# Kernel tuning notes

Hardware: AMD Instinct MI355X
Metric: run time of the kernel (lower is better)

The kernel has to match this reference:

```python
import jax, jax.numpy as jnp
import numpy as np

K_NN = 32          # configs['k']
LEAKY_ALPHA = 0.2  # configs['alpha']
NHEADS = 8         # all heads share gat_W0/gat_a0 in the weights dict -> tiled output
NEG_INF = -9e15    # masked-softmax fill used by dense GAT


@jax.custom_vjp
def grad_reverse(x):
    # GradientReversalLayer: identity forward, negated gradient backward
    return x

def _gr_fwd(x):
    return x, None

def _gr_bwd(res, g):
    return (-g,)

grad_reverse.defvjp(_gr_fwd, _gr_bwd)


def setup_inputs() -> dict:
    key = jax.random.key(0)
    ks = jax.random.split(key, 11)
    N, D = 6144, 512           # N = (num_domains+1)*batch_size = 4*1536
    H1, H2, G = 256, 128, 64   # hidden_layers=[256,128], gat_hidden=[64]
    C, ND = 16, 3              # num_classes, num source-domain discriminators

    def xav(k, shape):
        limit = np.float32(np.sqrt(6.0 / (shape[0] + shape[1])) * 1.414)
        return jax.random.uniform(k, shape, jnp.float32, -limit, limit)

    return {
        "x": jax.random.normal(ks[0], (N, D), jnp.float32),
        "fc_W0": xav(ks[1], (D, H1)),
        "fc_b0": jax.random.normal(ks[2], (H1,), jnp.float32) * 0.01,
        "fc_W1": xav(ks[3], (H1, H2)),
        "fc_b1": jax.random.normal(ks[4], (H2,), jnp.float32) * 0.01,
        "gat_W": xav(ks[5], (H2, G)),
        "gat_a": jax.random.normal(ks[6], (2 * G, 1), jnp.float32) * 0.1,
        "cls_W": xav(ks[7], (NHEADS * G, C)),
        "cls_b": jax.random.normal(ks[8], (C,), jnp.float32) * 0.01,
        "dsc_W": jax.random.uniform(ks[9], (ND, NHEADS * G, 2), jnp.float32),
        "dsc_b": jax.random.uniform(ks[10], (ND, 2), jnp.float32),
    }


def reference(x, fc_W0, fc_b0, fc_W1, fc_b1, gat_W, gat_a, cls_W, cls_b, dsc_W, dsc_b):
    # --- feature extractor MLP (Linear 'fc' + relu), dropout=0 / eval mode ---
    h = jax.nn.relu(x @ fc_W0 + fc_b0)
    h = jax.nn.relu(h @ fc_W1 + fc_b1)          # [N, 128]
    n = h.shape[0]

    # --- AdjacencyLayer / DistanceLayer: kNN over pairwise L2 distances ---
    sq = jnp.sum(h * h, axis=1)
    d2 = sq[:, None] + sq[None, :] - 2.0 * (h @ h.T)      # [N, N] squared dists
    d2 = d2 + jnp.eye(n, dtype=h.dtype) * 1e9             # exclude self from kNN
    _, idx = jax.lax.top_k(-jax.lax.stop_gradient(d2), K_NN)  # [N, K]
    adj = jnp.zeros((n, n), h.dtype).at[jnp.arange(n)[:, None], idx].set(1.0)
    adj = adj + jnp.eye(n, dtype=h.dtype)                 # self loops

    # --- dense GraphAttentionLayer (single shared head, tiled nheads times) ---
    Wh = h @ gat_W                                        # [N, G]
    Gd = Wh.shape[1]
    f1 = Wh @ gat_a[:Gd]                                  # [N, 1]
    f2 = Wh @ gat_a[Gd:]                                  # [N, 1]
    e = jax.nn.leaky_relu(f1 + f2.T, LEAKY_ALPHA)         # [N, N]
    att = jax.nn.softmax(jnp.where(adj > 0, e, NEG_INF), axis=1)
    hp = jax.nn.elu(att @ Wh)                             # [N, G]
    gat_out = jnp.tile(hp, (1, NHEADS))                   # concat of shared heads

    # --- class head + domain discriminators behind gradient reversal ---
    cls_logits = gat_out @ cls_W + cls_b                  # [N, C]
    rev = grad_reverse(gat_out)
    dsc_logits = jnp.einsum('nd,kdo->nko', rev, dsc_W) + dsc_b  # [N, ND, 2]
    return jnp.concatenate([cls_logits, dsc_logits.reshape(n, -1)], axis=1)
```

## Files before the change

### kernel.cpp

```cpp
#include <hip/hip_runtime.h>
#include <float.h>

#define N_PTS 6144
#define D_IN  512
#define H1_DIM 256
#define H2_DIM 128
#define G_DIM  64
#define KNN    32
#define NOUT   22
#define NQ     (N_PTS / 4)

typedef short s8v __attribute__((ext_vector_type(8)));
typedef float f32x4 __attribute__((ext_vector_type(4)));
typedef unsigned u32x4 __attribute__((ext_vector_type(4)));
typedef unsigned short u16;
typedef unsigned short u16x4 __attribute__((ext_vector_type(4)));
typedef unsigned long long u64;

__device__ __forceinline__ u16 f2bf(float f) {
  unsigned u = __float_as_uint(f);
  u += 0x7FFFu + ((u >> 16) & 1u);
  return (u16)(u >> 16);
}
__device__ __forceinline__ float bf2f(u16 s) {
  return __uint_as_float(((unsigned)s) << 16);
}
__device__ __forceinline__ void split3(float v, u16& a0, u16& a1, u16& a2) {
  a0 = f2bf(v);
  float r1 = v - bf2f(a0);
  a1 = f2bf(r1);
  a2 = f2bf(r1 - bf2f(a1));
}
__device__ __forceinline__ unsigned sortkey(float f) {
  unsigned ub = __float_as_uint(f);
  return (ub & 0x80000000u) ? ~ub : (ub | 0x80000000u);
}

template<int BM, bool AF32, bool SPLITK, bool BIAS, bool RELU, bool WF32, bool WSPLIT>
__global__ __launch_bounds__(256, 4) void mfma_gemm(
    const void* __restrict__ A0any, const u16* __restrict__ A1_, const u16* __restrict__ A2_,
    const u16* __restrict__ B0_, const u16* __restrict__ B1_, const u16* __restrict__ B2_,
    const float* __restrict__ bias,
    float* __restrict__ Cf, u16* __restrict__ C0, u16* __restrict__ C1, u16* __restrict__ C2,
    int Ktot, int Ks, int ldC, size_t MN)
{
  const int MT = BM / 32, NT = 2;
  const int APL = BM * 32;
  const int BBASE = 3 * APL;
  __shared__ u16 lds[(BM + 64) * 32 * 3];

  const int t = threadIdx.x;
  const int lane = t & 63, wave = t >> 6;
  const int wm = wave >> 1, wn = wave & 1;
  const int m0 = blockIdx.y * BM, n0 = blockIdx.x * 64;
  const int kz = blockIdx.z * Ks;

  f32x4 acc[MT][NT] = {};

  const int pA = BM / 16;
  const int NC = 3 * pA + 12;

  for (int k0 = 0; k0 < Ks; k0 += 32) {
    if (k0) __syncthreads();
    const int kb = kz + k0;
    if (AF32) {
      const float* A = (const float*)A0any;
      #pragma unroll
      for (int c0 = 0; c0 < BM * 4; c0 += 256) {
        int c = c0 + t;
        int row = c >> 2, slot = c & 3;
        const float* g = A + (size_t)(m0 + row) * Ktot + kb + slot * 8;
        f32x4 fa = *(const f32x4*)g;
        f32x4 fb = *(const f32x4*)(g + 4);
        int dst = row * 32 + ((slot ^ ((row >> 1) & 3)) << 3);
        s8v v0, v1, v2;
        #pragma unroll
        for (int e = 0; e < 4; ++e) {
          u16 a0, a1, a2; split3(fa[e], a0, a1, a2);
          v0[e] = (short)a0; v1[e] = (short)a1; v2[e] = (short)a2;
        }
        #pragma unroll
        for (int e = 0; e < 4; ++e) {
          u16 a0, a1, a2; split3(fb[e], a0, a1, a2);
          v0[4 + e] = (short)a0; v1[4 + e] = (short)a1; v2[4 + e] = (short)a2;
        }
        *(s8v*)(lds + dst) = v0;
        *(s8v*)(lds + APL + dst) = v1;
        *(s8v*)(lds + 2 * APL + dst) = v2;
      }
      for (int c = wave; c < 12; c += 4) {
        int p = c >> 2, lc = c & 3;
        int row = lc * 16 + (lane >> 2);
        int srcslot = (lane & 3) ^ ((row >> 1) & 3);
        const u16* src = (p == 0) ? B0_ : (p == 1) ? B1_ : B2_;
        const u16* g = src + (size_t)(n0 + row) * Ktot + kb + srcslot * 8;
        __builtin_amdgcn_global_load_lds(
            (const __attribute__((address_space(1))) unsigned*)g,
            (__attribute__((address_space(3))) unsigned*)(lds + BBASE + p * 2048 + lc * 512),
            16, 0, 0);
      }
    } else {
      for (int c = wave; c < NC; c += 4) {
        const u16* src; int dstoff; int row0; int lc;
        if (c < 3 * pA) {
          int p = c / pA; lc = c % pA;
          src = (p == 0) ? (const u16*)A0any : (p == 1) ? A1_ : A2_;
          dstoff = p * APL + lc * 512;
          row0 = m0;
        } else {
          int cb = c - 3 * pA;
          int p = cb >> 2; lc = cb & 3;
          src = (p == 0) ? B0_ : (p == 1) ? B1_ : B2_;
          dstoff = BBASE + p * 2048 + lc * 512;
          row0 = n0;
        }
        int row = lc * 16 + (lane >> 2);
        int srcslot = (lane & 3) ^ ((row >> 1) & 3);
        const u16* g = src + (size_t)(row0 + row) * Ktot + kb + srcslot * 8;
        __builtin_amdgcn_global_load_lds(
            (const __attribute__((address_space(1))) unsigned*)g,
            (__attribute__((address_space(3))) unsigned*)(lds + dstoff),
            16, 0, 0);
      }
    }
    __syncthreads();

    s8v af[3][MT], bf[3][NT];
    #pragma unroll
    for (int mt = 0; mt < MT; ++mt) {
      int r = wm * (BM / 2) + mt * 16 + (lane & 15);
      int off = r * 32 + (((lane >> 4) ^ ((r >> 1) & 3)) << 3);
      #pragma unroll
      for (int p = 0; p < 3; ++p) af[p][mt] = *(const s8v*)(lds + p * APL + off);
    }
    #pragma unroll
    for (int nt = 0; nt < NT; ++nt) {
      int r = wn * 32 + nt * 16 + (lane & 15);
      int off = r * 32 + (((lane >> 4) ^ ((r >> 1) & 3)) << 3);
      #pragma unroll
      for (int p = 0; p < 3; ++p) bf[p][nt] = *(const s8v*)(lds + BBASE + p * 2048 + off);
    }
    #pragma unroll
    for (int mt = 0; mt < MT; ++mt)
      #pragma unroll
      for (int nt = 0; nt < NT; ++nt) {
        f32x4 a = acc[mt][nt];
        a = __builtin_amdgcn_mfma_f32_16x16x32_bf16(af[0][mt], bf[0][nt], a, 0, 0, 0);
        a = __builtin_amdgcn_mfma_f32_16x16x32_bf16(af[0][mt], bf[1][nt], a, 0, 0, 0);
        a = __builtin_amdgcn_mfma_f32_16x16x32_bf16(af[1][mt], bf[0][nt], a, 0, 0, 0);
        a = __builtin_amdgcn_mfma_f32_16x16x32_bf16(af[1][mt], bf[1][nt], a, 0, 0, 0);
        a = __builtin_amdgcn_mfma_f32_16x16x32_bf16(af[0][mt], bf[2][nt], a, 0, 0, 0);
        a = __builtin_amdgcn_mfma_f32_16x16x32_bf16(af[2][mt], bf[0][nt], a, 0, 0, 0);
        acc[mt][nt] = a;
      }
  }

  #pragma unroll
  for (int mt = 0; mt < MT; ++mt) {
    #pragma unroll
    for (int nt = 0; nt < NT; ++nt) {
      int col = n0 + wn * 32 + nt * 16 + (lane & 15);
      float bv = (BIAS && !SPLITK) ? bias[col] : 0.f;
      #pragma unroll
      for (int v = 0; v < 4; ++v) {
        int row = m0 + wm * (BM / 2) + mt * 16 + (lane >> 4) * 4 + v;
        float val = acc[mt][nt][v] + bv;
        size_t o = (size_t)row * ldC + col;
        if (SPLITK) {
          Cf[(size_t)blockIdx.z * MN + o] = val;
        } else {
          if (RELU) val = fmaxf(val, 0.f);
          if (WF32) Cf[o] = val;
          if (WSPLIT) {
            u16 a0, a1, a2; split3(val, a0, a1, a2);
            C0[o] = a0; C1[o] = a1; C2[o] = a2;
          }
        }
      }
    }
  }
}

__global__ __launch_bounds__(512, 4) void gram_symm(
    const u16* __restrict__ A0, const u16* __restrict__ A1, const u16* __restrict__ A2,
    const float* __restrict__ sq, u16* __restrict__ Ck, u16* __restrict__ Qm, int ldC)
{
  if ((int)blockIdx.x < (int)blockIdx.y) return;
  const int MT = 4, NT = 2;
  __shared__ u16 lds[2 * 128 * 32 * 3];

  const int t = threadIdx.x;
  const int lane = t & 63, wave = t >> 6;
  const int wm = wave >> 2, wn = wave & 3;
  const int m0 = blockIdx.y * 128, n0 = blockIdx.x * 128;
  const bool mirror = (int)blockIdx.x > (int)blockIdx.y;

  f32x4 acc[MT][NT] = {};

  for (int k0 = 0; k0 < H2_DIM; k0 += 32) {
    if (k0) __syncthreads();
    for (int c = wave; c < 48; c += 8) {
      int half = c >= 24;
      int cb = half ? c - 24 : c;
      int p = cb >> 3, lc = cb & 7;
      const u16* src = (p == 0) ? A0 : (p == 1) ? A1 : A2;
      int dstoff = half * 12288 + p * 4096 + lc * 512;
      int row0 = half ? n0 : m0;
      int row = lc * 16 + (lane >> 2);
      int srcslot = (lane & 3) ^ ((row >> 1) & 3);
      const u16* g = src + (size_t)(row0 + row) * H2_DIM + k0 + srcslot * 8;
      __builtin_amdgcn_global_load_lds(
          (const __attribute__((address_space(1))) unsigned*)g,
          (__attribute__((address_space(3))) unsigned*)(lds + dstoff),
          16, 0, 0);
    }
    __syncthreads();

    s8v af[3][MT], bf[3][NT];
    #pragma unroll
    for (int mt = 0; mt < MT; ++mt) {
      int r = wm * 64 + mt * 16 + (lane & 15);
      int off = r * 32 + (((lane >> 4) ^ ((r >> 1) & 3)) << 3);
      #pragma unroll
      for (int p = 0; p < 3; ++p) af[p][mt] = *(const s8v*)(lds + p * 4096 + off);
    }
    #pragma unroll
    for (int nt = 0; nt < NT; ++nt) {
      int r = wn * 32 + nt * 16 + (lane & 15);
      int off = r * 32 + (((lane >> 4) ^ ((r >> 1) & 3)) << 3);
      #pragma unroll
      for (int p = 0; p < 3; ++p) bf[p][nt] = *(const s8v*)(lds + 12288 + p * 4096 + off);
    }
    #pragma unroll
    for (int mt = 0; mt < MT; ++mt)
      #pragma unroll
      for (int nt = 0; nt < NT; ++nt) {
        f32x4 a = acc[mt][nt];
        a = __builtin_amdgcn_mfma_f32_16x16x32_bf16(af[0][mt], bf[0][nt], a, 0, 0, 0);
        a = __builtin_amdgcn_mfma_f32_16x16x32_bf16(af[0][mt], bf[1][nt], a, 0, 0, 0);
        a = __builtin_amdgcn_mfma_f32_16x16x32_bf16(af[1][mt], bf[0][nt], a, 0, 0, 0);
        a = __builtin_amdgcn_mfma_f32_16x16x32_bf16(af[1][mt], bf[1][nt], a, 0, 0, 0);
        a = __builtin_amdgcn_mfma_f32_16x16x32_bf16(af[0][mt], bf[2][nt], a, 0, 0, 0);
        a = __builtin_amdgcn_mfma_f32_16x16x32_bf16(af[2][mt], bf[0][nt], a, 0, 0, 0);
        acc[mt][nt] = a;
      }
  }

  unsigned mk32[MT][NT][2];
  __syncthreads();
  u16* stD = lds;
  #pragma unroll
  for (int mt = 0; mt < MT; ++mt) {
    #pragma unroll
    for (int nt = 0; nt < NT; ++nt) {
      int cl = wn * 32 + nt * 16 + (lane & 15);
      float sqc = sq[n0 + cl];
      #pragma unroll
      for (int v = 0; v < 4; ++v) {
        int rl = wm * 64 + mt * 16 + (lane >> 4) * 4 + v;
        float val = acc[mt][nt][v];
        float f = fmaf(-2.f, val, sqc);
        unsigned uu = sortkey(f);
        if (m0 + rl == n0 + cl) uu = 0xFFFFFFFFu;
        stD[rl * 136 + cl] = (u16)(uu >> 16);
        if (mirror) {
          unsigned km = sortkey(fmaf(-2.f, val, sq[m0 + rl])) >> 16;
          if (v & 1) mk32[mt][nt][v >> 1] |= km << 16;
          else       mk32[mt][nt][v >> 1] = km;
        }
      }
    }
  }
  __syncthreads();
  for (int e = t; e < 128 * 16; e += 512) {
    int row = e >> 4, ch = e & 15;
    u32x4 vv = *(const u32x4*)(stD + row * 136 + ch * 8);
    *(u32x4*)(Ck + (size_t)(m0 + row) * ldC + n0 + ch * 8) = vv;
  }
  for (int e = t; e < 128 * 32; e += 512) {
    int row = e >> 5, qg = e & 31;
    const u16* p = stD + row * 136 + qg * 4;
    u16 a = p[0] < p[1] ? p[0] : p[1];
    u16 b = p[2] < p[3] ? p[2] : p[3];
    Qm[(size_t)(m0 + row) * NQ + (n0 >> 2) + qg] = a < b ? a : b;
  }
  if (mirror) {
    __syncthreads();
    u16* stM = lds;
    #pragma unroll
    for (int mt = 0; mt < MT; ++mt) {
      #pragma unroll
      for (int nt = 0; nt < NT; ++nt) {
        int cl = wn * 32 + nt * 16 + (lane & 15);
        #pragma unroll
        for (int v = 0; v < 4; ++v) {
          int rl = wm * 64 + mt * 16 + (lane >> 4) * 4 + v;
          unsigned km = (v & 1) ? (mk32[mt][nt][v >> 1] >> 16)
                                : (mk32[mt][nt][v >> 1] & 0xFFFFu);
          stM[cl * 136 + rl] = (u16)km;
        }
      }
    }
    __syncthreads();
    for (int e = t; e < 128 * 16; e += 512) {
      int row = e >> 4, ch = e & 15;
      u32x4 vv = *(const u32x4*)(stM + row * 136 + ch * 8);
      *(u32x4*)(Ck + (size_t)(n0 + row) * ldC + m0 + ch * 8) = vv;
    }
    for (int e = t; e < 128 * 32; e += 512) {
      int row = e >> 5, qg = e & 31;
      const u16* p = stM + row * 136 + qg * 4;
      u16 a = p[0] < p[1] ? p[0] : p[1];
      u16 b = p[2] < p[3] ? p[2] : p[3];
      Qm[(size_t)(n0 + row) * NQ + (m0 >> 2) + qg] = a < b ? a : b;
    }
  }
}

template<int S, bool BIAS, bool RELU, bool WF32, bool WSPLIT>
__global__ void combine(const float* __restrict__ P, const float* __restrict__ bias,
                        size_t MN, int Ncols,
                        float* __restrict__ Cf, u16* __restrict__ C0,
                        u16* __restrict__ C1, u16* __restrict__ C2)
{
  size_t idx = ((size_t)blockIdx.x * 256 + threadIdx.x) * 4;
  if (idx >= MN) return;
  f32x4 s = *(const f32x4*)(P + idx);
  #pragma unroll
  for (int z = 1; z < S; ++z) s += *(const f32x4*)(P + (size_t)z * MN + idx);
  int n = (int)(idx % (size_t)Ncols);
  #pragma unroll
  for (int e = 0; e < 4; ++e) {
    float v = s[e] + (BIAS ? bias[n + e] : 0.f);
    if (RELU) v = fmaxf(v, 0.f);
    if (WF32) Cf[idx + e] = v;
    if (WSPLIT) {
      u16 a0, a1, a2; split3(v, a0, a1, a2);
      C0[idx + e] = a0; C1[idx + e] = a1; C2[idx + e] = a2;
    }
  }
}

__global__ void prep_all(const float* __restrict__ W0, u16* __restrict__ a0,
                         u16* __restrict__ a1, u16* __restrict__ a2,
                         const float* __restrict__ W1, u16* __restrict__ b0,
                         u16* __restrict__ b1, u16* __restrict__ b2,
                         const float* __restrict__ gW, u16* __restrict__ c0,
                         u16* __restrict__ c1, u16* __restrict__ c2,
                         const float* __restrict__ cW, const float* __restrict__ cb,
                         const float* __restrict__ dW, const float* __restrict__ db,
                         float* __restrict__ Wc, float* __restrict__ bc)
{
  int id = blockIdx.x * 256 + threadIdx.x;
  const int S0 = D_IN * H1_DIM, S1 = H1_DIM * H2_DIM, S2 = H2_DIM * G_DIM;
  const int SW = S0 + S1 + S2;
  if (id < SW) {
    const float* W; u16 *p0, *p1, *p2; int K, N;
    if (id < S0)           { W = W0; p0 = a0; p1 = a1; p2 = a2; K = D_IN;   N = H1_DIM; }
    else if (id < S0 + S1) { id -= S0; W = W1; p0 = b0; p1 = b1; p2 = b2; K = H1_DIM; N = H2_DIM; }
    else                   { id -= S0 + S1; W = gW; p0 = c0; p1 = c1; p2 = c2; K = H2_DIM; N = G_DIM; }
    int k = id / N, n = id % N;
    u16 x0, x1, x2;
    split3(W[id], x0, x1, x2);
    size_t o = (size_t)n * K + k;
    p0[o] = x0; p1[o] = x1; p2[o] = x2;
    return;
  }
  id -= SW;
  if (id < 64 * NOUT) {
    int g = id / NOUT, c = id % NOUT;
    float s = 0.f;
    if (c < 16) {
      for (int r = 0; r < 8; ++r) s += cW[(r * 64 + g) * 16 + c];
    } else {
      int k = (c - 16) >> 1, o = (c - 16) & 1;
      for (int r = 0; r < 8; ++r) s += dW[k * 1024 + (r * 64 + g) * 2 + o];
    }
    Wc[id] = s;
    if (g == 0) bc[c] = (c < 16) ? cb[c] : db[c - 16];
  }
}

__global__ void row_stats(const float* __restrict__ h, const float* __restrict__ Wh,
                          const float* __restrict__ ga, float* __restrict__ sq,
                          float* __restrict__ f1, float* __restrict__ f2)
{
  int i = blockIdx.x * 256 + threadIdx.x;
  const float* hr = h + (size_t)i * H2_DIM;
  float s = 0.f;
  for (int k = 0; k < H2_DIM; ++k) { float v = hr[k]; s = fmaf(v, v, s); }
  sq[i] = s;
  const float* wr = Wh + (size_t)i * G_DIM;
  float a = 0.f, b = 0.f;
  for (int g = 0; g < G_DIM; ++g) {
    float w = wr[g];
    a = fmaf(w, ga[g], a);
    b = fmaf(w, ga[G_DIM + g], b);
  }
  f1[i] = a; f2[i] = b;
}

__global__ __launch_bounds__(256) void topk_att(const u16* __restrict__ Sb,
    const u16* __restrict__ Qm,
    const float* __restrict__ f1, const float* __restrict__ f2,
    const float* __restrict__ Wh, const float* __restrict__ Wc, const float* __restrict__ bc,
    const float* __restrict__ sq, const float* __restrict__ hF,
    float* __restrict__ out, int m0, int nrows)
{
  const int t = threadIdx.x;
  const int lane = t & 63, wv = t >> 6;
  const int row4 = (nrows - 4 - blockIdx.x * 4) + wv;
  const int i = m0 + row4;
  const u16* Srow = Sb + (size_t)row4 * N_PTS;
  const u16* Qrow = Qm + (size_t)row4 * NQ;

  __shared__ float WcL[64 * NOUT];
  __shared__ unsigned candS[4][384];
  __shared__ u16 tieS[4][128];
  __shared__ float hiL[4][128];
  __shared__ int neighS[4][33];
  __shared__ float attS[4][33];
  __shared__ float hpfS[4][64];

  for (int idx = t; idx < 64 * NOUT; idx += 256) WcL[idx] = Wc[idx];
  __syncthreads();

  hiL[wv][lane]      = hF[(size_t)i * H2_DIM + lane];
  hiL[wv][64 + lane] = hF[(size_t)i * H2_DIM + 64 + lane];

  unsigned q[24];
  #pragma unroll
  for (int g = 0; g < 6; ++g) {
    u16x4 v = *(const u16x4*)(Qrow + (g << 8) + (lane << 2));
    #pragma unroll
    for (int e = 0; e < 4; ++e) q[g * 4 + e] = (unsigned)v[e];
  }
  #define QI(s) (((s >> 2) << 8) + (lane << 2) + (s & 3))

  unsigned lmin = q[0];
  #pragma unroll
  for (int c = 1; c < 24; ++c) lmin = q[c] < lmin ? q[c] : lmin;

  unsigned mnl = lmin, mxl = lmin;
  #pragma unroll
  for (int off = 32; off > 0; off >>= 1) {
    unsigned o1 = __shfl_xor(mnl, off); mnl = o1 < mnl ? o1 : mnl;
    unsigned o2 = __shfl_xor(mxl, off); mxl = o2 > mxl ? o2 : mxl;
  }

  long long lo = (long long)mnl - 1, hi = (long long)mxl;
  while (hi - lo > 1) {
    long long span = hi - lo;
    unsigned m1 = (unsigned)(lo + (span >> 2));
    unsigned m2 = (unsigned)(lo + (span >> 1));
    unsigned m3 = (unsigned)(hi - (span >> 2));
    int c1 = 0, c2 = 0, c3 = 0;
    #pragma unroll
    for (int c = 0; c < 24; ++c) {
      c1 += (q[c] <= m1);
      c2 += (q[c] <= m2);
      c3 += (q[c] <= m3);
    }
    #pragma unroll
    for (int off = 32; off > 0; off >>= 1) {
      c1 += __shfl_xor(c1, off);
      c2 += __shfl_xor(c2, off);
      c3 += __shfl_xor(c3, off);
    }
    if (c1 >= KNN)       { hi = m1; }
    else if (c2 >= KNN)  { lo = m1; hi = m2; }
    else if (c3 >= KNN)  { lo = m2; hi = m3; }
    else                 { lo = m3; }
  }
  const unsigned Q = (unsigned)hi;

  #pragma unroll
  for (int s = 0; s < 6; ++s) candS[wv][lane + s * 64] = 0xFFFFFFFFu;
  const u64 below = (lane == 0) ? 0ull : (~0ull >> (64 - lane));
  int qcnt = 0;
  #pragma unroll
  for (int s = 0; s < 24; ++s) {
    bool act = (q[s] <= Q);
    u64 mask = __ballot(act);
    if (act) {
      int pos = qcnt + (int)__popcll(mask & below);
      if (pos < 96) {
        int qi = QI(s);
        u16x4 v = *(const u16x4*)(Srow + (qi << 2));
        #pragma unroll
        for (int e = 0; e < 4; ++e) {
          int j = (qi << 2) + e;
          candS[wv][pos * 4 + e] = ((unsigned)v[e] << 13) | (unsigned)j;
        }
      }
    }
    qcnt += (int)__popcll(mask);
  }

  unsigned ck[6];
  #pragma unroll
  for (int s = 0; s < 6; ++s) ck[s] = candS[wv][lane + s * 64];

  lo = -1; hi = 0x10000;
  while (hi - lo > 1) {
    long long span = hi - lo;
    unsigned m1 = (unsigned)(lo + (span >> 2));
    unsigned m2 = (unsigned)(lo + (span >> 1));
    unsigned m3 = (unsigned)(hi - (span >> 2));
    int c1 = 0, c2 = 0, c3 = 0;
    #pragma unroll
    for (int s = 0; s < 6; ++s) {
      unsigned k = ck[s] >> 13;
      c1 += (k <= m1);
      c2 += (k <= m2);
      c3 += (k <= m3);
    }
    #pragma unroll
    for (int off = 32; off > 0; off >>= 1) {
      c1 += __shfl_xor(c1, off);
      c2 += __shfl_xor(c2, off);
      c3 += __shfl_xor(c3, off);
    }
    if (c1 >= KNN)       { hi = m1; }
    else if (c2 >= KNN)  { lo = m1; hi = m2; }
    else if (c3 >= KNN)  { lo = m2; hi = m3; }
    else                 { lo = m3; }
  }
  const unsigned T = (unsigned)hi;

  int sA = 0, sB = 0;
  #pragma unroll
  for (int s = 0; s < 6; ++s) {
    unsigned k = ck[s] >> 13;
    bool strict = (k < T);
    u64 ms = __ballot(strict);
    if (strict) {
      int pos = sA + (int)__popcll(ms & below);
      if (pos < 32) neighS[wv][pos] = (int)(ck[s] & 0x1FFFu);
    }
    sA += (int)__popcll(ms);
    bool tie = (k == T);
    u64 mt2 = __ballot(tie);
    if (tie) {
      int pos = sB + (int)__popcll(mt2 & below);
      if (pos < 128) tieS[wv][pos] = (u16)(ck[s] & 0x1FFFu);
    }
    sB += (int)__popcll(mt2);
  }
  if (sB > 128) sB = 128;
  const int need = KNN - sA;

  u64 r0 = ~0ull, r1 = ~0ull;
  const float* hi0 = &hiL[wv][0];
  #pragma unroll
  for (int half = 0; half < 2; ++half) {
    int e = lane + half * 64;
    if (e < sB) {
      int j = tieS[wv][e];
      const float* hj = hF + (size_t)j * H2_DIM;
      float dot = 0.f;
      for (int d = 0; d < H2_DIM; d += 4) {
        f32x4 a = *(const f32x4*)(hi0 + d);
        f32x4 b = *(const f32x4*)(hj + d);
        dot = fmaf(a[0], b[0], fmaf(a[1], b[1], fmaf(a[2], b[2], fmaf(a[3], b[3], dot))));
      }
      float f = fmaf(-2.f, dot, sq[j]);
      u64 rk = ((u64)sortkey(f) << 13) | (unsigned)j;
      if (half == 0) r0 = rk; else r1 = rk;
    }
  }

  {
    candS[wv][lane] = (unsigned)(r0 >> 32); candS[wv][64 + lane] = (unsigned)r0;
    candS[wv][128 + lane] = (unsigned)(r1 >> 32); candS[wv][192 + lane] = (unsigned)r1;
    u64 v0 = ((u64)candS[wv][(2 * lane) >= 64 ? 128 + (2 * lane - 64) : 2 * lane] << 32)
           | candS[wv][(2 * lane) >= 64 ? 192 + (2 * lane - 64) : 64 + 2 * lane];
    u64 v1 = ((u64)candS[wv][(2 * lane + 1) >= 64 ? 128 + (2 * lane + 1 - 64) : 2 * lane + 1] << 32)
           | candS[wv][(2 * lane + 1) >= 64 ? 192 + (2 * lane + 1 - 64) : 64 + 2 * lane + 1];
    const int e0 = 2 * lane, e1 = e0 + 1;
    for (int k = 2; k <= 128; k <<= 1) {
      for (int j = k >> 1; j >= 2; j >>= 1) {
        int half = j >> 1;
        u64 o0 = __shfl_xor(v0, half);
        u64 o1 = __shfl_xor(v1, half);
        bool up0 = ((e0 & k) == 0) == ((e0 & j) == 0);
        bool up1 = ((e1 & k) == 0) == ((e1 & j) == 0);
        v0 = up0 ? (v0 < o0 ? v0 : o0) : (v0 > o0 ? v0 : o0);
        v1 = up1 ? (v1 < o1 ? v1 : o1) : (v1 > o1 ? v1 : o1);
      }
      bool asc = ((e0 & k) == 0);
      u64 a = v0 < v1 ? v0 : v1, b = v0 < v1 ? v1 : v0;
      v0 = asc ? a : b;
      v1 = asc ? b : a;
    }
    if (e0 < need) neighS[wv][sA + e0] = (int)(v0 & 0x1FFFu);
    if (e1 < need) neighS[wv][sA + e1] = (int)(v1 & 0x1FFFu);
  }
  if (lane == 0) neighS[wv][32] = i;

  {
    float e = -FLT_MAX;
    if (lane < 33) {
      float raw = f1[i] + f2[neighS[wv][lane]];
      e = raw > 0.f ? raw : 0.2f * raw;
    }
    float mx = e;
    #pragma unroll
    for (int off = 32; off > 0; off >>= 1) mx = fmaxf(mx, __shfl_xor(mx, off));
    float ex = (lane < 33) ? expf(e - mx) : 0.f;
    float sm = ex;
    #pragma unroll
    for (int off = 32; off > 0; off >>= 1) sm += __shfl_xor(sm, off);
    if (lane < 33) attS[wv][lane] = ex / sm;
  }

  {
    float s = 0.f;
    for (int m = 0; m < 33; ++m)
      s = fmaf(attS[wv][m], Wh[(size_t)neighS[wv][m] * G_DIM + lane], s);
    hpfS[wv][lane] = s > 0.f ? s : expm1f(s);
  }

  if (lane < NOUT) {
    float o = bc[lane];
    for (int g = 0; g < 64; ++g) o = fmaf(hpfS[wv][g], WcL[g * NOUT + lane], o);
    out[(size_t)i * NOUT + lane] = o;
  }
}

extern "C" void kernel_launch(void* const* d_in, const int* in_sizes, int n_in,
                              void* d_out, int out_size, void* d_ws, size_t ws_size,
                              hipStream_t stream)
{
  const float* x  = (const float*)d_in[0];
  const float* W0 = (const float*)d_in[1];
  const float* b0 = (const float*)d_in[2];
  const float* W1 = (const float*)d_in[3];
  const float* b1 = (const float*)d_in[4];
  const float* gW = (const float*)d_in[5];
  const float* ga = (const float*)d_in[6];
  const float* cW = (const float*)d_in[7];
  const float* cb = (const float*)d_in[8];
  const float* dW = (const float*)d_in[9];
  const float* db = (const float*)d_in[10];
  float* out = (float*)d_out;

  char* base = (char*)d_ws;
  char* w = base;
  auto alloc = [&](size_t bytes) { char* p = w; w += (bytes + 255) & ~(size_t)255; return p; };
  u16 *W0p[3], *W1p[3], *gWp[3], *h1p[3], *hp[3];
  for (int p = 0; p < 3; ++p) W0p[p] = (u16*)alloc((size_t)D_IN * H1_DIM * 2);
  for (int p = 0; p < 3; ++p) W1p[p] = (u16*)alloc((size_t)H1_DIM * H2_DIM * 2);
  for (int p = 0; p < 3; ++p) gWp[p] = (u16*)alloc((size_t)H2_DIM * G_DIM * 2);
  for (int p = 0; p < 3; ++p) h1p[p] = (u16*)alloc((size_t)N_PTS * H1_DIM * 2);
  for (int p = 0; p < 3; ++p) hp[p]  = (u16*)alloc((size_t)N_PTS * H2_DIM * 2);
  float* hF  = (float*)alloc((size_t)N_PTS * H2_DIM * 4);
  float* WhF = (float*)alloc((size_t)N_PTS * G_DIM * 4);
  float* sqv = (float*)alloc(N_PTS * 4);
  float* f1v = (float*)alloc(N_PTS * 4);
  float* f2v = (float*)alloc(N_PTS * 4);
  float* Wc  = (float*)alloc(64 * NOUT * 4);
  float* bc  = (float*)alloc(64 * 4);
  u16* Qm    = (u16*)alloc((size_t)N_PTS * NQ * 2);

  char* pbase = w;
  const size_t MN1 = (size_t)N_PTS * H1_DIM;
  const size_t MN2 = (size_t)N_PTS * H2_DIM;
  const size_t MN3 = (size_t)N_PTS * G_DIM;
  float* P1 = (float*)alloc(4 * MN1 * 4);
  float* P2 = (float*)alloc(4 * MN2 * 4);
  float* P3 = (float*)alloc(4 * MN3 * 4);
  u16* Sb = (u16*)pbase;

  const int TS = D_IN * H1_DIM + H1_DIM * H2_DIM + H2_DIM * G_DIM + 64 * NOUT;
  prep_all<<<(TS + 255) / 256, 256, 0, stream>>>(
      W0, W0p[0], W0p[1], W0p[2], W1, W1p[0], W1p[1], W1p[2], gW, gWp[0], gWp[1], gWp[2],
      cW, cb, dW, db, Wc, bc);

  mfma_gemm<64, true, true, false, false, false, false>
      <<<dim3(H1_DIM / 64, N_PTS / 64, 4), 256, 0, stream>>>(
      x, nullptr, nullptr, W0p[0], W0p[1], W0p[2], nullptr,
      P1, nullptr, nullptr, nullptr, D_IN, D_IN / 4, H1_DIM, MN1);
  combine<4, true, true, false, true><<<(int)(MN1 / 1024), 256, 0, stream>>>(
      P1, b0, MN1, H1_DIM, nullptr, h1p[0], h1p[1], h1p[2]);

  mfma_gemm<64, false, true, false, false, false, false>
      <<<dim3(H2_DIM / 64, N_PTS / 64, 4), 256, 0, stream>>>(
      h1p[0], h1p[1], h1p[2], W1p[0], W1p[1], W1p[2], nullptr,
      P2, nullptr, nullptr, nullptr, H1_DIM, H1_DIM / 4, H2_DIM, MN2);
  combine<4, true, true, true, true><<<(int)(MN2 / 1024), 256, 0, stream>>>(
      P2, b1, MN2, H2_DIM, hF, hp[0], hp[1], hp[2]);

  mfma_gemm<64, false, true, false, false, false, false>
      <<<dim3(G_DIM / 64, N_PTS / 64, 4), 256, 0, stream>>>(
      hp[0], hp[1], hp[2], gWp[0], gWp[1], gWp[2], nullptr,
      P3, nullptr, nullptr, nullptr, H2_DIM, H2_DIM / 4, G_DIM, MN3);
  combine<4, false, false, true, false><<<(int)(MN3 / 1024), 256, 0, stream>>>(
      P3, nullptr, MN3, G_DIM, WhF, nullptr, nullptr, nullptr);

  row_stats<<<N_PTS / 256, 256, 0, stream>>>(hF, WhF, ga, sqv, f1v, f2v);

  gram_symm<<<dim3(N_PTS / 128, N_PTS / 128), 512, 0, stream>>>(
      hp[0], hp[1], hp[2], sqv, Sb, Qm, N_PTS);
  topk_att<<<N_PTS / 4, 256, 0, stream>>>(Sb, Qm, f1v, f2v, WhF, Wc, bc, sqv, hF, out, 0, N_PTS);
}
```

Baseline: 161.5 us.

## Tighten kNN threshold search range, skip tie sort, and halve first GEMM split-K

Before the binary search for the kNN key threshold, a wave-wide min/max reduction over the candidate keys narrows the initial search range, so fewer iterations are needed. When the number of ties exactly matches the remaining slots, the tie rescoring and bitonic sort are skipped and the ties are copied directly. The tie dot product now uses four independent accumulators to shorten the dependency chain. The first MLP GEMM drops from a 4-way to a 2-way split-K, which halves the partial buffer and the combine traffic but leaves less parallelism per output tile.

```diff
diff --git a/kernel.cpp b/kernel.cpp
--- a/kernel.cpp
+++ b/kernel.cpp
@@ -501,7 +501,22 @@
   #pragma unroll
   for (int s = 0; s < 6; ++s) ck[s] = candS[wv][lane + s * 64];
 
-  lo = -1; hi = 0x10000;
+  unsigned kmn = 0x10000u, kmx = 0u;
+  #pragma unroll
+  for (int s = 0; s < 6; ++s) {
+    unsigned k = ck[s] >> 13;
+    if (k <= 0xFFFFu) {
+      kmn = k < kmn ? k : kmn;
+      kmx = k > kmx ? k : kmx;
+    }
+  }
+  #pragma unroll
+  for (int off = 32; off > 0; off >>= 1) {
+    unsigned o1 = __shfl_xor(kmn, off); kmn = o1 < kmn ? o1 : kmn;
+    unsigned o2 = __shfl_xor(kmx, off); kmx = o2 > kmx ? o2 : kmx;
+  }
+
+  lo = (long long)kmn - 1; hi = (long long)kmx;
   while (hi - lo > 1) {
     long long span = hi - lo;
     unsigned m1 = (unsigned)(lo + (span >> 2));
@@ -550,27 +565,39 @@
   if (sB > 128) sB = 128;
   const int need = KNN - sA;
 
-  u64 r0 = ~0ull, r1 = ~0ull;
-  const float* hi0 = &hiL[wv][0];
-  #pragma unroll
-  for (int half = 0; half < 2; ++half) {
-    int e = lane + half * 64;
-    if (e < sB) {
-      int j = tieS[wv][e];
-      const float* hj = hF + (size_t)j * H2_DIM;
-      float dot = 0.f;
-      for (int d = 0; d < H2_DIM; d += 4) {
-        f32x4 a = *(const f32x4*)(hi0 + d);
-        f32x4 b = *(const f32x4*)(hj + d);
-        dot = fmaf(a[0], b[0], fmaf(a[1], b[1], fmaf(a[2], b[2], fmaf(a[3], b[3], dot))));
-      }
-      float f = fmaf(-2.f, dot, sq[j]);
-      u64 rk = ((u64)sortkey(f) << 13) | (unsigned)j;
-      if (half == 0) r0 = rk; else r1 = rk;
-    }
-  }
-
-  {
+  if (sB == need) {
+    if (lane < need) neighS[wv][sA + lane] = tieS[wv][lane];
+  } else {
+    u64 r0 = ~0ull, r1 = ~0ull;
+    const float* hi0 = &hiL[wv][0];
+    #pragma unroll
+    for (int half = 0; half < 2; ++half) {
+      int e = lane + half * 64;
+      if (e < sB) {
+        int j = tieS[wv][e];
+        const float* hj = hF + (size_t)j * H2_DIM;
+        float d0 = 0.f, d1 = 0.f, d2 = 0.f, d3 = 0.f;
+        for (int d = 0; d < H2_DIM; d += 16) {
+          f32x4 a0 = *(const f32x4*)(hi0 + d);
+          f32x4 b0 = *(const f32x4*)(hj + d);
+          f32x4 a1 = *(const f32x4*)(hi0 + d + 4);
+          f32x4 b1 = *(const f32x4*)(hj + d + 4);
+          f32x4 a2 = *(const f32x4*)(hi0 + d + 8);
+          f32x4 b2 = *(const f32x4*)(hj + d + 8);
+          f32x4 a3 = *(const f32x4*)(hi0 + d + 12);
+          f32x4 b3 = *(const f32x4*)(hj + d + 12);
+          d0 = fmaf(a0[0], b0[0], fmaf(a0[1], b0[1], fmaf(a0[2], b0[2], fmaf(a0[3], b0[3], d0))));
+          d1 = fmaf(a1[0], b1[0], fmaf(a1[1], b1[1], fmaf(a1[2], b1[2], fmaf(a1[3], b1[3], d1))));
+          d2 = fmaf(a2[0], b2[0], fmaf(a2[1], b2[1], fmaf(a2[2], b2[2], fmaf(a2[3], b2[3], d2))));
+          d3 = fmaf(a3[0], b3[0], fmaf(a3[1], b3[1], fmaf(a3[2], b3[2], fmaf(a3[3], b3[3], d3))));
+        }
+        float dot = (d0 + d1) + (d2 + d3);
+        float f = fmaf(-2.f, dot, sq[j]);
+        u64 rk = ((u64)sortkey(f) << 13) | (unsigned)j;
+        if (half == 0) r0 = rk; else r1 = rk;
+      }
+    }
+
     candS[wv][lane] = (unsigned)(r0 >> 32); candS[wv][64 + lane] = (unsigned)r0;
     candS[wv][128 + lane] = (unsigned)(r1 >> 32); candS[wv][192 + lane] = (unsigned)r1;
     u64 v0 = ((u64)candS[wv][(2 * lane) >= 64 ? 128 + (2 * lane - 64) : 2 * lane] << 32)
@@ -667,7 +694,7 @@
   const size_t MN1 = (size_t)N_PTS * H1_DIM;
   const size_t MN2 = (size_t)N_PTS * H2_DIM;
   const size_t MN3 = (size_t)N_PTS * G_DIM;
-  float* P1 = (float*)alloc(4 * MN1 * 4);
+  float* P1 = (float*)alloc(2 * MN1 * 4);
   float* P2 = (float*)alloc(4 * MN2 * 4);
   float* P3 = (float*)alloc(4 * MN3 * 4);
   u16* Sb = (u16*)pbase;
@@ -678,10 +705,10 @@
       cW, cb, dW, db, Wc, bc);
 
   mfma_gemm<64, true, true, false, false, false, false>
-      <<<dim3(H1_DIM / 64, N_PTS / 64, 4), 256, 0, stream>>>(
+      <<<dim3(H1_DIM / 64, N_PTS / 64, 2), 256, 0, stream>>>(
       x, nullptr, nullptr, W0p[0], W0p[1], W0p[2], nullptr,
-      P1, nullptr, nullptr, nullptr, D_IN, D_IN / 4, H1_DIM, MN1);
-  combine<4, true, true, false, true><<<(int)(MN1 / 1024), 256, 0, stream>>>(
+      P1, nullptr, nullptr, nullptr, D_IN, D_IN / 2, H1_DIM, MN1);
+  combine<2, true, true, false, true><<<(int)(MN1 / 1024), 256, 0, stream>>>(
       P1, b0, MN1, H1_DIM, nullptr, h1p[0], h1p[1], h1p[2]);
 
   mfma_gemm<64, false, true, false, false, false, false>
```

Result: no change. 162.7 us (+0.7%).
